# Kernel tuning notes

Measured on AMD Instinct MI355X. Metric: run time of the kernel, lower is better.

## Reference

```python
import jax, jax.numpy as jnp
import numpy as np

DSIZE = 1024
STRIDES = [8, 16, 32]
FSIZES = [(128, 128), (64, 64), (32, 32)]
LAYOUTS = [[16, 32], [64, 128], [256, 512]]
IOU_THR = 0.3
B, M = 16, 128


def _gen_anchors():
    # replicates BBoxAnchors.generate_anchors: anchors in (cx, cy, w, h)
    outs = []
    for stride, (fw, fh), layout in zip(STRIDES, FSIZES, LAYOUTS):
        lay = np.array([[0.0, 0.0, float(w), float(w)] for w in layout], dtype=np.float32)  # [k,4]
        vx = np.arange(0.5, fw, dtype=np.float32) * stride
        vy = np.arange(0.5, fh, dtype=np.float32) * stride
        gy, gx = np.meshgrid(vy, vx, indexing='ij')
        off = np.stack([gx, gy], axis=-1)  # [fh,fw,2]
        a = np.broadcast_to(lay, (fh, fw, len(layout), 4)).copy()
        a[..., :2] += off[:, :, None, :]
        outs.append(a.reshape(-1, 4))
    return np.concatenate(outs, axis=0)  # [A,4]


def cbox2bbox(c):
    return jnp.concatenate([c[..., :2] - c[..., 2:] * 0.5, c[..., :2] + c[..., 2:] * 0.5], axis=-1)


def box_iou_pairwise(a, b):
    # a: [A,4] xyxy, b: [M,4] xyxy -> [A,M]
    lt = jnp.maximum(a[:, None, :2], b[None, :, :2])
    rb = jnp.minimum(a[:, None, 2:], b[None, :, 2:])
    wh = jnp.clip(rb - lt, 0.0)
    inter = wh[..., 0] * wh[..., 1]
    area_a = (a[:, 2] - a[:, 0]) * (a[:, 3] - a[:, 1])
    area_b = (b[:, 2] - b[:, 0]) * (b[:, 3] - b[:, 1])
    return inter / (area_a[:, None] + area_b[None, :] - inter)


def _match(banchors, labels, bboxes):
    iou = box_iou_pairwise(banchors, bboxes)  # [A,M]
    max_iou_of_anchor = iou.max(axis=1)
    box_indice = iou.argmax(axis=1)
    max_iou_of_bbox = iou.max(axis=0)
    anchor_indice = iou.argmax(axis=0)

    def body(carry, xs):
        mioa, bi = carry
        j, a, v = xs
        return (mioa.at[a].set(v), bi.at[a].set(j)), None

    (max_iou_of_anchor, box_indice), _ = jax.lax.scan(
        body, (max_iou_of_anchor, box_indice),
        (jnp.arange(M, dtype=box_indice.dtype), anchor_indice, max_iou_of_bbox))

    denom = jnp.maximum(max_iou_of_bbox, IOU_THR)[box_indice]
    max_iou_of_anchor = jnp.where(max_iou_of_anchor < IOU_THR * 0.5, 0.0, max_iou_of_anchor)
    scores = max_iou_of_anchor / denom
    scores = jnp.where(labels[box_indice] <= 0, 0.0, scores)
    return scores, box_indice


def setup_inputs() -> dict:
    key = jax.random.key(0)
    k1, k2, k3 = jax.random.split(key, 3)
    labels = jax.random.randint(k1, (B, M), 0, 5, dtype=jnp.int32)
    cxy = jax.random.uniform(k2, (B, M, 2), dtype=jnp.float32) * DSIZE
    wh = jax.random.uniform(k3, (B, M, 2), dtype=jnp.float32) * 248.0 + 8.0
    bboxes = jnp.concatenate([cxy - wh * 0.5, cxy + wh * 0.5], axis=-1)  # xyxy
    anchors = jnp.asarray(_gen_anchors())  # [43008,4] cxcywh
    return {"labels": labels, "bboxes": bboxes, "anchors": anchors}


def reference(labels, bboxes, anchors):
    banchors = cbox2bbox(anchors)  # [A,4]
    scores, bi = jax.vmap(lambda l, b: _match(banchors, l, b))(labels, bboxes)  # [B,A],[B,A]
    matched = jnp.take_along_axis(bboxes, bi[..., None], axis=1)  # [B,A,4]
    return scores, matched
```

## Files before the change

### kernel.cpp

```cpp
#include <hip/hip_runtime.h>
#include <stdint.h>

typedef unsigned long long u64;

#define A_TOTAL 43008
#define NB 16
#define NM 128
#define SPLIT 168
#define WPB 4

__device__ __forceinline__ float exact_div(float x, float y) {
    float r;
    asm("v_rcp_f32 %0, %1" : "=v"(r) : "v"(y));
    float e  = __builtin_fmaf(-y, r, 1.0f);
    r        = __builtin_fmaf(e, r, r);
    e        = __builtin_fmaf(-y, r, 1.0f);
    r        = __builtin_fmaf(e, r, r);
    float q  = x * r;
    float rs = __builtin_fmaf(-y, q, x);
    return __builtin_fmaf(rs, r, q);
}

__device__ __forceinline__ u64 dpp_u64(u64 v, const int ctrl) {
    int lo = (int)(unsigned)v, hi = (int)(unsigned)(v >> 32);
    int plo, phi;
    switch (ctrl) {
        case 0xB1:
            plo = __builtin_amdgcn_update_dpp(lo, lo, 0xB1, 0xF, 0xF, false);
            phi = __builtin_amdgcn_update_dpp(hi, hi, 0xB1, 0xF, 0xF, false);
            break;
        case 0x4E:
            plo = __builtin_amdgcn_update_dpp(lo, lo, 0x4E, 0xF, 0xF, false);
            phi = __builtin_amdgcn_update_dpp(hi, hi, 0x4E, 0xF, 0xF, false);
            break;
        default:
            plo = __builtin_amdgcn_update_dpp(lo, lo, 0x141, 0xF, 0xF, false);
            phi = __builtin_amdgcn_update_dpp(hi, hi, 0x141, 0xF, 0xF, false);
            break;
    }
    return ((u64)(unsigned)phi << 32) | (unsigned)plo;
}

__global__ __launch_bounds__(256) void prep_kernel(
    const float4* __restrict__ bboxes, float* __restrict__ areaBp,
    u64* __restrict__ colfinal, float4* __restrict__ chunkbnd) {
#pragma clang fp contract(off)
    const int i = blockIdx.x * 256 + threadIdx.x;
    float4 v = bboxes[i];
    areaBp[i] = (v.z - v.x) * (v.w - v.y);
    colfinal[i] = 0ull;
    if (blockIdx.x == 0) {
        const int t = threadIdx.x;
        const int base = (t >> 4) * NM + (t & 15) * 8;
        float4 f = bboxes[base];
        float mnx = f.x, mny = f.y, mxx = f.z, mxy = f.w;
#pragma unroll
        for (int k = 1; k < 8; ++k) {
            float4 u = bboxes[base + k];
            mnx = fminf(mnx, u.x); mny = fminf(mny, u.y);
            mxx = fmaxf(mxx, u.z); mxy = fmaxf(mxy, u.w);
        }
        chunkbnd[t] = make_float4(mnx, mny, mxx, mxy);
    }
}

__global__ __launch_bounds__(256) void fused_kernel(
    const float4* __restrict__ anchors, const float* __restrict__ bb,
    const float* __restrict__ areaBp, const float4* __restrict__ chunkbnd,
    u64* __restrict__ rowkey,
    u64* __restrict__ colfinal) {
#pragma clang fp contract(off)
    const int b = blockIdx.y, tid = threadIdx.x;
    const int lane = tid & 63, wv = tid >> 6;
    const int abase = blockIdx.x * 256 + wv * 64;

    __shared__ float s_col[WPB][8][65];
    __shared__ u64   s_ck[WPB][NM];

    s_ck[wv][lane] = 0ull;
    s_ck[wv][64 + lane] = 0ull;

    float4 an = anchors[abase + lane];
    float hw = an.z * 0.5f, hh = an.w * 0.5f;
    float ax1 = an.x - hw, ay1 = an.y - hh;
    float ax2 = an.x + hw, ay2 = an.y + hh;
    float areaA = (ax2 - ax1) * (ay2 - ay1);

    const float* box  = bb + (size_t)b * NM * 4;
    const float* area = areaBp + (size_t)b * NM;
    const float4* cb  = chunkbnd + (b << 4);

    float best_v = 0.0f; int best_m = 0;
    const int bi = lane >> 3, part = lane & 7;
    const int rbase = part * 8;

    for (int c = 0; c < 16; ++c) {
        float4 g = cb[c];
        bool cl = (g.z > ax1) & (g.x < ax2) & (g.w > ay1) & (g.y < ay2);
        if (__ballot(cl) == 0ull) continue;

        unsigned mask = 0;
#pragma unroll
        for (int i = 0; i < 8; ++i) {
            const int m = c * 8 + i;
            const float bx1 = box[4 * m + 0], by1 = box[4 * m + 1];
            const float bx2 = box[4 * m + 2], by2 = box[4 * m + 3];
            bool lv = (bx2 > ax1) & (bx1 < ax2) & (by2 > ay1) & (by1 < ay2);
            if (__ballot(lv) != 0ull) {
                mask |= 1u << i;
                const float areaB = area[m];
                float ltx = fmaxf(ax1, bx1), lty = fmaxf(ay1, by1);
                float rbx = fminf(ax2, bx2), rby = fminf(ay2, by2);
                float wx = fmaxf(rbx - ltx, 0.0f), wy = fmaxf(rby - lty, 0.0f);
                float inter = wx * wy;
                float iou = exact_div(inter, (areaA + areaB) - inter);
                if (iou > best_v) { best_v = iou; best_m = m; }
                s_col[wv][i][lane] = iou;
            }
        }
        if (mask == 0u) continue;

        u64 key = 0ull;
        if (mask & (1u << bi)) {
            float v = -1.0f; int tb = 0;
#pragma unroll
            for (int t = 0; t < 8; ++t) {
                float o = s_col[wv][bi][rbase + t];
                if (o > v) { v = o; tb = t; }
            }
            unsigned aidx = (unsigned)(abase + rbase + tb);
            key = ((u64)__float_as_uint(v) << 32) | (u64)(unsigned)(~aidx);
        }
        { u64 o = dpp_u64(key, 0xB1);  if (o > key) key = o; }
        { u64 o = dpp_u64(key, 0x4E);  if (o > key) key = o; }
        { u64 o = dpp_u64(key, 0x141); if (o > key) key = o; }
        if (part == 0) s_ck[wv][c * 8 + bi] = key;
    }

    rowkey[(size_t)b * A_TOTAL + abase + lane] =
        ((u64)__float_as_uint(best_v) << 32) | (u64)(unsigned)best_m;

    __syncthreads();
    if (tid < NM) {
        u64 k = s_ck[0][tid];
        for (int w = 1; w < WPB; ++w) if (s_ck[w][tid] > k) k = s_ck[w][tid];
        atomicMax(&colfinal[b * NM + tid], k);
    }
}

__global__ __launch_bounds__(256) void epilogue_kernel(
    const float4* __restrict__ bboxes, const int* __restrict__ labels,
    const u64* __restrict__ colfinal, const u64* __restrict__ rowkey,
    float* __restrict__ out_scores, float4* __restrict__ out_matched) {
#pragma clang fp contract(off)
    const int b = blockIdx.y, tid = threadIdx.x;
    const int a0 = blockIdx.x * 256, a = a0 + tid;

    __shared__ float4 sbox[NM];
    __shared__ float  s_cm[NM];
    __shared__ int    s_lab[NM];
    __shared__ int    ovr[256];
    ovr[tid] = -1;

    int my_ca = -1;
    if (tid < NM) {
        u64 k = colfinal[b * NM + tid];
        s_cm[tid] = __uint_as_float((unsigned)(k >> 32));
        my_ca = ~((int)(unsigned)(k & 0xFFFFFFFFull));
        sbox[tid]  = bboxes[b * NM + tid];
        s_lab[tid] = labels[b * NM + tid];
    }
    __syncthreads();
    if (tid < NM && my_ca >= a0 && my_ca < a0 + 256)
        atomicMax(&ovr[my_ca - a0], tid);
    __syncthreads();

    u64 rk = rowkey[(size_t)b * A_TOTAL + a];
    float best = __uint_as_float((unsigned)(rk >> 32));
    int   bi   = (int)(rk & 0xFFFFFFFFull);

    int o = ovr[tid];
    if (o >= 0) { bi = o; best = s_cm[o]; }

    float denom = fmaxf(s_cm[bi], 0.3f);
    float val   = (best < 0.15f) ? 0.0f : best;
    float score = val / denom;
    if (s_lab[bi] <= 0) score = 0.0f;

    out_scores[(size_t)b * A_TOTAL + a]  = score;
    out_matched[(size_t)b * A_TOTAL + a] = sbox[bi];
}

extern "C" void kernel_launch(void* const* d_in, const int* in_sizes, int n_in,
                              void* d_out, int out_size, void* d_ws, size_t ws_size,
                              hipStream_t stream) {
    const int*    labels  = (const int*)d_in[0];
    const float4* bboxes  = (const float4*)d_in[1];
    const float4* anchors = (const float4*)d_in[2];

    float* out = (float*)d_out;

    char* ws = (char*)d_ws;
    u64*    rowkey   = (u64*)ws;                     ws += (size_t)NB * A_TOTAL * 8;
    u64*    colfinal = (u64*)ws;                     ws += (size_t)NB * NM * 8;
    float*  areaBp   = (float*)ws;                   ws += (size_t)NB * NM * 4;
    float4* chunkbnd = (float4*)ws;

    prep_kernel<<<(NB * NM) / 256, 256, 0, stream>>>(bboxes, areaBp, colfinal,
                                                     chunkbnd);

    dim3 g(SPLIT, NB);
    fused_kernel<<<g, 256, 0, stream>>>(anchors, (const float*)bboxes, areaBp,
                                        chunkbnd, rowkey, colfinal);
    epilogue_kernel<<<g, 256, 0, stream>>>(
        bboxes, labels, colfinal, rowkey,
        out, (float4*)(out + (size_t)NB * A_TOTAL));
}
```

Measured before the change: 105.2 us.

## Use persistent workers with atomic work queue ordered largest-anchors-first

Replaces the fixed 2D grid of the IoU kernel with a persistent grid of 2048 blocks. Each block grabs groups of wave-sized units (64 anchors times one batch image) from a global atomic counter. Units are issued in reverse anchor order so the large-anchor waves, which overlap many boxes and do the most work, start first. This is meant to fix load imbalance across blocks. Per-column maxima now go directly to global atomicMax per wave instead of a block-level shared reduction, which adds global atomic traffic and a block-wide sync per work fetch.

Result: slower. 172.6 us (+64.1%).

```diff
diff --git a/kernel.cpp b/kernel.cpp
--- a/kernel.cpp
+++ b/kernel.cpp
@@ -8,6 +8,8 @@
 #define NM 128
 #define SPLIT 168
 #define WPB 4
+#define NUNITS (NB * 672)
+#define NWORKERS 2048
 
 __device__ __forceinline__ float exact_div(float x, float y) {
     float r;
@@ -43,12 +45,14 @@
 
 __global__ __launch_bounds__(256) void prep_kernel(
     const float4* __restrict__ bboxes, float* __restrict__ areaBp,
-    u64* __restrict__ colfinal, float4* __restrict__ chunkbnd) {
+    u64* __restrict__ colfinal, float4* __restrict__ chunkbnd,
+    int* __restrict__ wcnt) {
 #pragma clang fp contract(off)
     const int i = blockIdx.x * 256 + threadIdx.x;
     float4 v = bboxes[i];
     areaBp[i] = (v.z - v.x) * (v.w - v.y);
     colfinal[i] = 0ull;
+    if (i == 0) *wcnt = 0;
     if (blockIdx.x == 0) {
         const int t = threadIdx.x;
         const int base = (t >> 4) * NM + (t & 15) * 8;
@@ -68,83 +72,86 @@
     const float4* __restrict__ anchors, const float* __restrict__ bb,
     const float* __restrict__ areaBp, const float4* __restrict__ chunkbnd,
     u64* __restrict__ rowkey,
-    u64* __restrict__ colfinal) {
+    u64* __restrict__ colfinal,
+    int* __restrict__ wcnt) {
 #pragma clang fp contract(off)
-    const int b = blockIdx.y, tid = threadIdx.x;
+    const int tid = threadIdx.x;
     const int lane = tid & 63, wv = tid >> 6;
-    const int abase = blockIdx.x * 256 + wv * 64;
-
-    __shared__ float s_col[WPB][8][65];
-    __shared__ u64   s_ck[WPB][NM];
-
-    s_ck[wv][lane] = 0ull;
-    s_ck[wv][64 + lane] = 0ull;
-
-    float4 an = anchors[abase + lane];
-    float hw = an.z * 0.5f, hh = an.w * 0.5f;
-    float ax1 = an.x - hw, ay1 = an.y - hh;
-    float ax2 = an.x + hw, ay2 = an.y + hh;
-    float areaA = (ax2 - ax1) * (ay2 - ay1);
-
-    const float* box  = bb + (size_t)b * NM * 4;
-    const float* area = areaBp + (size_t)b * NM;
-    const float4* cb  = chunkbnd + (b << 4);
-
-    float best_v = 0.0f; int best_m = 0;
     const int bi = lane >> 3, part = lane & 7;
     const int rbase = part * 8;
 
-    for (int c = 0; c < 16; ++c) {
-        float4 g = cb[c];
-        bool cl = (g.z > ax1) & (g.x < ax2) & (g.w > ay1) & (g.y < ay2);
-        if (__ballot(cl) == 0ull) continue;
-
-        unsigned mask = 0;
+    __shared__ float s_col[WPB][8][65];
+    __shared__ int   s_u;
+
+    for (;;) {
+        __syncthreads();
+        if (tid == 0) s_u = atomicAdd(wcnt, WPB);
+        __syncthreads();
+        const int base = s_u;
+        if (base >= NUNITS) break;
+        const int u = base + wv;
+        const int w = 671 - (u >> 4);
+        const int b = u & 15;
+        const int abase = w * 64;
+
+        float4 an = anchors[abase + lane];
+        float hw = an.z * 0.5f, hh = an.w * 0.5f;
+        float ax1 = an.x - hw, ay1 = an.y - hh;
+        float ax2 = an.x + hw, ay2 = an.y + hh;
+        float areaA = (ax2 - ax1) * (ay2 - ay1);
+
+        const float* box  = bb + (size_t)b * NM * 4;
+        const float* area = areaBp + (size_t)b * NM;
+        const float4* cb  = chunkbnd + (b << 4);
+
+        float best_v = 0.0f; int best_m = 0;
+
+        for (int c = 0; c < 16; ++c) {
+            float4 g = cb[c];
+            bool cl = (g.z > ax1) & (g.x < ax2) & (g.w > ay1) & (g.y < ay2);
+            if (__ballot(cl) == 0ull) continue;
+
+            unsigned mask = 0;
 #pragma unroll
-        for (int i = 0; i < 8; ++i) {
-            const int m = c * 8 + i;
-            const float bx1 = box[4 * m + 0], by1 = box[4 * m + 1];
-            const float bx2 = box[4 * m + 2], by2 = box[4 * m + 3];
-            bool lv = (bx2 > ax1) & (bx1 < ax2) & (by2 > ay1) & (by1 < ay2);
-            if (__ballot(lv) != 0ull) {
-                mask |= 1u << i;
-                const float areaB = area[m];
-                float ltx = fmaxf(ax1, bx1), lty = fmaxf(ay1, by1);
-                float rbx = fminf(ax2, bx2), rby = fminf(ay2, by2);
-                float wx = fmaxf(rbx - ltx, 0.0f), wy = fmaxf(rby - lty, 0.0f);
-                float inter = wx * wy;
-                float iou = exact_div(inter, (areaA + areaB) - inter);
-                if (iou > best_v) { best_v = iou; best_m = m; }
-                s_col[wv][i][lane] = iou;
+            for (int i = 0; i < 8; ++i) {
+                const int m = c * 8 + i;
+                const float bx1 = box[4 * m + 0], by1 = box[4 * m + 1];
+                const float bx2 = box[4 * m + 2], by2 = box[4 * m + 3];
+                bool lv = (bx2 > ax1) & (bx1 < ax2) & (by2 > ay1) & (by1 < ay2);
+                if (__ballot(lv) != 0ull) {
+                    mask |= 1u << i;
+                    const float areaB = area[m];
+                    float ltx = fmaxf(ax1, bx1), lty = fmaxf(ay1, by1);
+                    float rbx = fminf(ax2, bx2), rby = fminf(ay2, by2);
+                    float wx = fmaxf(rbx - ltx, 0.0f), wy = fmaxf(rby - lty, 0.0f);
+                    float inter = wx * wy;
+                    float iou = exact_div(inter, (areaA + areaB) - inter);
+                    if (iou > best_v) { best_v = iou; best_m = m; }
+                    s_col[wv][i][lane] = iou;
+                }
             }
+            if (mask == 0u) continue;
+
+            u64 key = 0ull;
+            if (mask & (1u << bi)) {
+                float v = -1.0f; int tb = 0;
+#pragma unroll
+                for (int t = 0; t < 8; ++t) {
+                    float o = s_col[wv][bi][rbase + t];
+                    if (o > v) { v = o; tb = t; }
+                }
+                unsigned aidx = (unsigned)(abase + rbase + tb);
+                key = ((u64)__float_as_uint(v) << 32) | (u64)(unsigned)(~aidx);
+            }
+            { u64 o = dpp_u64(key, 0xB1);  if (o > key) key = o; }
+            { u64 o = dpp_u64(key, 0x4E);  if (o > key) key = o; }
+            { u64 o = dpp_u64(key, 0x141); if (o > key) key = o; }
+            if (part == 0 && key)
+                atomicMax(&colfinal[b * NM + c * 8 + bi], key);
         }
-        if (mask == 0u) continue;
-
-        u64 key = 0ull;
-        if (mask & (1u << bi)) {
-            float v = -1.0f; int tb = 0;
-#pragma unroll
-            for (int t = 0; t < 8; ++t) {
-                float o = s_col[wv][bi][rbase + t];
-                if (o > v) { v = o; tb = t; }
-            }
-            unsigned aidx = (unsigned)(abase + rbase + tb);
-            key = ((u64)__float_as_uint(v) << 32) | (u64)(unsigned)(~aidx);
-        }
-        { u64 o = dpp_u64(key, 0xB1);  if (o > key) key = o; }
-        { u64 o = dpp_u64(key, 0x4E);  if (o > key) key = o; }
-        { u64 o = dpp_u64(key, 0x141); if (o > key) key = o; }
-        if (part == 0) s_ck[wv][c * 8 + bi] = key;
-    }
-
-    rowkey[(size_t)b * A_TOTAL + abase + lane] =
-        ((u64)__float_as_uint(best_v) << 32) | (u64)(unsigned)best_m;
-
-    __syncthreads();
-    if (tid < NM) {
-        u64 k = s_ck[0][tid];
-        for (int w = 1; w < WPB; ++w) if (s_ck[w][tid] > k) k = s_ck[w][tid];
-        atomicMax(&colfinal[b * NM + tid], k);
+
+        rowkey[(size_t)b * A_TOTAL + abase + lane] =
+            ((u64)__float_as_uint(best_v) << 32) | (u64)(unsigned)best_m;
     }
 }
 
@@ -204,14 +211,16 @@
     u64*    rowkey   = (u64*)ws;                     ws += (size_t)NB * A_TOTAL * 8;
     u64*    colfinal = (u64*)ws;                     ws += (size_t)NB * NM * 8;
     float*  areaBp   = (float*)ws;                   ws += (size_t)NB * NM * 4;
-    float4* chunkbnd = (float4*)ws;
+    float4* chunkbnd = (float4*)ws;                  ws += (size_t)NB * 16 * 16;
+    int*    wcnt     = (int*)ws;
 
     prep_kernel<<<(NB * NM) / 256, 256, 0, stream>>>(bboxes, areaBp, colfinal,
-                                                     chunkbnd);
+                                                     chunkbnd, wcnt);
+
+    fused_kernel<<<dim3(NWORKERS), 256, 0, stream>>>(
+        anchors, (const float*)bboxes, areaBp, chunkbnd, rowkey, colfinal, wcnt);
 
     dim3 g(SPLIT, NB);
-    fused_kernel<<<g, 256, 0, stream>>>(anchors, (const float*)bboxes, areaBp,
-                                        chunkbnd, rowkey, colfinal);
     epilogue_kernel<<<g, 256, 0, stream>>>(
         bboxes, labels, colfinal, rowkey,
         out, (float4*)(out + (size_t)NB * A_TOTAL));
```

## Reschedule IoU kernel as per-wave units with reversed order and direct atomics

Applied to the files above, without the earlier changes.

The fused IoU kernel now uses 128-thread blocks that each process two independent 64-anchor wave units. Units are enumerated in reverse anchor order, so the heavy large-anchor waves (which overlap many boxes) launch first and load balance better. The per-block shared-memory column reduction and its barrier are removed, and each wave issues global atomicMax for non-empty column keys directly, which may raise atomic traffic. Chunk-overlap ballots are precomputed into a bitmask so the loop only iterates over active chunks.

New measurement: 146.5 us. 39.3% more time.

```diff
diff --git a/kernel.cpp b/kernel.cpp
--- a/kernel.cpp
+++ b/kernel.cpp
@@ -7,7 +7,9 @@
 #define NB 16
 #define NM 128
 #define SPLIT 168
-#define WPB 4
+#define NUNITS (NB * 672)
+#define UPB 2
+#define NBLK (NUNITS / UPB)
 
 __device__ __forceinline__ float exact_div(float x, float y) {
     float r;
@@ -64,21 +66,23 @@
     }
 }
 
-__global__ __launch_bounds__(256) void fused_kernel(
+__global__ __launch_bounds__(128) void fused_kernel(
     const float4* __restrict__ anchors, const float* __restrict__ bb,
     const float* __restrict__ areaBp, const float4* __restrict__ chunkbnd,
     u64* __restrict__ rowkey,
     u64* __restrict__ colfinal) {
 #pragma clang fp contract(off)
-    const int b = blockIdx.y, tid = threadIdx.x;
+    const int tid = threadIdx.x;
     const int lane = tid & 63, wv = tid >> 6;
-    const int abase = blockIdx.x * 256 + wv * 64;
-
-    __shared__ float s_col[WPB][8][65];
-    __shared__ u64   s_ck[WPB][NM];
-
-    s_ck[wv][lane] = 0ull;
-    s_ck[wv][64 + lane] = 0ull;
+    const int bi = lane >> 3, part = lane & 7;
+    const int rbase = part * 8;
+
+    __shared__ float s_col[UPB][8][65];
+
+    const int g = blockIdx.x * UPB + wv;
+    const int w = 671 - (g >> 4);
+    const int b = g & 15;
+    const int abase = w * 64;
 
     float4 an = anchors[abase + lane];
     float hw = an.z * 0.5f, hh = an.w * 0.5f;
@@ -90,14 +94,19 @@
     const float* area = areaBp + (size_t)b * NM;
     const float4* cb  = chunkbnd + (b << 4);
 
+    unsigned cmask = 0;
+#pragma unroll
+    for (int c = 0; c < 16; ++c) {
+        float4 gb = cb[c];
+        bool cl = (gb.z > ax1) & (gb.x < ax2) & (gb.w > ay1) & (gb.y < ay2);
+        if (__ballot(cl) != 0ull) cmask |= 1u << c;
+    }
+
     float best_v = 0.0f; int best_m = 0;
-    const int bi = lane >> 3, part = lane & 7;
-    const int rbase = part * 8;
-
-    for (int c = 0; c < 16; ++c) {
-        float4 g = cb[c];
-        bool cl = (g.z > ax1) & (g.x < ax2) & (g.w > ay1) & (g.y < ay2);
-        if (__ballot(cl) == 0ull) continue;
+
+    while (cmask) {
+        const int c = __builtin_ctz(cmask);
+        cmask &= cmask - 1;
 
         unsigned mask = 0;
 #pragma unroll
@@ -134,18 +143,12 @@
         { u64 o = dpp_u64(key, 0xB1);  if (o > key) key = o; }
         { u64 o = dpp_u64(key, 0x4E);  if (o > key) key = o; }
         { u64 o = dpp_u64(key, 0x141); if (o > key) key = o; }
-        if (part == 0) s_ck[wv][c * 8 + bi] = key;
+        if (part == 0 && key)
+            atomicMax(&colfinal[b * NM + c * 8 + bi], key);
     }
 
     rowkey[(size_t)b * A_TOTAL + abase + lane] =
         ((u64)__float_as_uint(best_v) << 32) | (u64)(unsigned)best_m;
-
-    __syncthreads();
-    if (tid < NM) {
-        u64 k = s_ck[0][tid];
-        for (int w = 1; w < WPB; ++w) if (s_ck[w][tid] > k) k = s_ck[w][tid];
-        atomicMax(&colfinal[b * NM + tid], k);
-    }
 }
 
 __global__ __launch_bounds__(256) void epilogue_kernel(
@@ -209,9 +212,10 @@
     prep_kernel<<<(NB * NM) / 256, 256, 0, stream>>>(bboxes, areaBp, colfinal,
                                                      chunkbnd);
 
+    fused_kernel<<<dim3(NBLK), 128, 0, stream>>>(
+        anchors, (const float*)bboxes, areaBp, chunkbnd, rowkey, colfinal);
+
     dim3 g(SPLIT, NB);
-    fused_kernel<<<g, 256, 0, stream>>>(anchors, (const float*)bboxes, areaBp,
-                                        chunkbnd, rowkey, colfinal);
     epilogue_kernel<<<g, 256, 0, stream>>>(
         bboxes, labels, colfinal, rowkey,
         out, (float4*)(out + (size_t)NB * A_TOTAL));
```
